# Kernel tuning notes

Hardware: AMD Instinct MI355X
Metric: run time of the kernel (lower is better)

Reference implementation:

```python
import jax, jax.numpy as jnp
import numpy as np
from jax import lax

N_ITERS = 32     # fixed iteration count (random graph diameter << 32, converges)
NEG = -1e9       # finite stand-in for -inf so grads stay finite


def _seg_logsumexp(x, seg, n):
    # numerically stable log-sum-exp scatter over segments (per-node over out-edges)
    m = jax.ops.segment_max(x, seg, num_segments=n)
    m = jnp.maximum(m, NEG)  # empty segments give -inf -> floor at NEG
    s = jax.ops.segment_sum(jnp.exp(x - m[seg]), seg, num_segments=n)
    return jnp.where(s > 0, jnp.log(s) + m, NEG)


def setup_inputs() -> dict:
    key = jax.random.key(0)
    k1, k2 = jax.random.split(key)
    N, E, F = 50000, 1600000, 64
    # scaled uniform features -> edge utilities ~ -7.4 mean => contraction, VI converges
    feats = jax.random.uniform(k1, (E, F), dtype=jnp.float32) * 0.2
    edge_index = jax.random.randint(k2, (2, E), 0, N)
    dest_mask = (jnp.arange(N) % 100) == 0  # 500 destination nodes
    batch = jnp.zeros((N,), dtype=jnp.int32)  # single graph (unused by VI solver)
    weight = jnp.full((1, F), -1.0, dtype=jnp.float32)  # module's constant init
    bias = jnp.full((1,), -1.0, dtype=jnp.float32)
    return {"feats": feats, "dest_mask": dest_mask, "edge_index": edge_index,
            "batch": batch, "n_nodes": N, "weight": weight, "bias": bias}


def reference(feats, dest_mask, edge_index, batch, n_nodes, weight, bias):
    # util = clamp(Linear(feats), -100, -1e-6), shape [E, 1]
    util = jnp.clip(feats @ weight.T + bias, -100.0, -1e-6)
    u = util[:, 0]                      # [E]
    src, dst = edge_index[0], edge_index[1]

    # value iteration: V(i) = LSE_{e: src(e)=i} (u_e + V(dst_e)), V(dest) = 0
    v0 = jnp.where(dest_mask, 0.0, NEG)

    def step(v, _):
        v_new = _seg_logsumexp(u + v[dst], src, n_nodes)
        v_new = jnp.where(dest_mask, 0.0, v_new)
        return v_new, None

    value, _ = lax.scan(step, v0, None, length=N_ITERS)  # [N]

    # edge choice probability: P(e) = exp(u_e + V(dst_e) - V(src_e))
    prob = jnp.exp(u + value[dst] - value[src])          # [E]
    return value, util, prob
```

## Files before the change

kernel.cpp:

```cpp
#include <hip/hip_runtime.h>

#define NEGV (-1000000000.0f)
#define N_ITERS 32
#define NBUCK 512
#define B1 256
#define REG 4096
#define CPAD 16

typedef float f32x4 __attribute__((ext_vector_type(4)));

__global__ __launch_bounds__(256) void util_kernel64gs(
    const float* __restrict__ feats, const float* __restrict__ weight,
    const float* __restrict__ bias, float* __restrict__ u,
    int* __restrict__ cursors, int* __restrict__ flags, int E)
{
    if (blockIdx.x == 0) {
        for (int i = threadIdx.x; i < NBUCK; i += 256)
            cursors[(size_t)i * CPAD] = i * REG;
        if (threadIdx.x <= N_ITERS)
            flags[threadIdx.x] = (threadIdx.x <= 1) ? 1 : 0;
    }
    int tid = blockIdx.x * blockDim.x + threadIdx.x;
    int l = tid & 15;
    int g = tid >> 4;
    int ngroups = (gridDim.x * blockDim.x) >> 4;
    f32x4 wv = *reinterpret_cast<const f32x4*>(weight + l * 4);
    float bb = bias[0];
    for (int e = g; e < E; e += ngroups) {
        f32x4 fv = __builtin_nontemporal_load(
            reinterpret_cast<const f32x4*>(feats + (size_t)e * 64 + l * 4));
        float s = fv.x * wv.x + fv.y * wv.y + fv.z * wv.z + fv.w * wv.w;
        s += __shfl_xor(s, 8, 16);
        s += __shfl_xor(s, 4, 16);
        s += __shfl_xor(s, 2, 16);
        s += __shfl_xor(s, 1, 16);
        if (l == 0)
            u[e] = fminf(fmaxf(s + bb, -100.0f), -1e-6f);
    }
}

__global__ __launch_bounds__(256) void util_kernel(
    const float* __restrict__ feats, const float* __restrict__ weight,
    const float* __restrict__ bias, float* __restrict__ u,
    int* __restrict__ cursors, int* __restrict__ flags, int E, int F)
{
    if (blockIdx.x == 0) {
        for (int i = threadIdx.x; i < NBUCK; i += 256)
            cursors[(size_t)i * CPAD] = i * REG;
        if (threadIdx.x <= N_ITERS)
            flags[threadIdx.x] = (threadIdx.x <= 1) ? 1 : 0;
    }
    int e = blockIdx.x * blockDim.x + threadIdx.x;
    if (e >= E) return;
    const float* row = feats + (size_t)e * (size_t)F;
    float acc = 0.0f;
    for (int f = 0; f < F; f += 4) {
        float4 fv = *reinterpret_cast<const float4*>(row + f);
        acc += fv.x * weight[f + 0];
        acc += fv.y * weight[f + 1];
        acc += fv.z * weight[f + 2];
        acc += fv.w * weight[f + 3];
    }
    acc += bias[0];
    u[e] = fminf(fmaxf(acc, -100.0f), -1e-6f);
}

__global__ __launch_bounds__(256) void scatter_fused(
    const int* __restrict__ src, const int* __restrict__ dst,
    const float* __restrict__ u, int* __restrict__ cursors,
    int2* __restrict__ edg, int E, int W, int chunk)
{
    __shared__ int h[NBUCK];
    for (int i = threadIdx.x; i < NBUCK; i += 256) h[i] = 0;
    __syncthreads();
    const int lo = blockIdx.x * chunk;
    const int hi = min(E, lo + chunk);
    for (int e = lo + threadIdx.x; e < hi; e += 256)
        atomicAdd(&h[(unsigned)src[e] / (unsigned)W], 1);
    __syncthreads();
    for (int k = threadIdx.x; k < NBUCK; k += 256) {
        int c = h[k];
        h[k] = (c > 0) ? atomicAdd(&cursors[(size_t)k * CPAD], c) : 0;
    }
    __syncthreads();
    for (int e = lo + threadIdx.x; e < hi; e += 256) {
        int s = src[e];
        unsigned k = (unsigned)s / (unsigned)W;
        int pos = atomicAdd(&h[k], 1);
        if (pos < (int)((k + 1) * REG)) {
            unsigned sl = (unsigned)s - k * (unsigned)W;
            int2 rec;
            rec.x = (int)((sl << 20) | (unsigned)dst[e]);
            rec.y = __float_as_int(expf(u[e]));
            edg[pos] = rec;
        }
    }
}

__global__ __launch_bounds__(256) void fine_sort(
    const int* __restrict__ cursors, int2* __restrict__ edg,
    int* __restrict__ row_ptr, int* __restrict__ row_end,
    const int* __restrict__ dest_mask, float* __restrict__ ew1,
    int N, int W)
{
    __shared__ int pks[REG];
    __shared__ int ubs[REG];
    __shared__ int fh[132];
    __shared__ int rst[132];

    const int k  = blockIdx.x;
    const int lo = k * W;
    const int nn = min(N, lo + W) - lo;
    if (nn <= 0) return;

    const int bs = k * REG;
    int cnt = cursors[(size_t)k * CPAD] - bs;
    if (cnt > REG) cnt = REG;
    if (cnt < 0) cnt = 0;

    for (int i = threadIdx.x; i < cnt; i += 256) {
        int2 r = edg[bs + i];
        pks[i] = r.x;
        ubs[i] = r.y;
    }
    for (int i = threadIdx.x; i < nn; i += 256) fh[i] = 0;
    __syncthreads();

    for (int i = threadIdx.x; i < cnt; i += 256)
        atomicAdd(&fh[((unsigned)pks[i]) >> 20], 1);
    __syncthreads();

    if (threadIdx.x == 0) {
        int run = bs;
        for (int i = 0; i < nn; ++i) {
            int c = fh[i];
            fh[i] = run;
            rst[i] = run;
            row_ptr[lo + i] = run;
            row_end[lo + i] = run + c;
            run += c;
        }
    }
    __syncthreads();

    for (int i = threadIdx.x; i < cnt; i += 256) {
        int w = pks[i];
        int pos = atomicAdd(&fh[((unsigned)w) >> 20], 1);
        int2 r;
        r.x = w & 0xFFFFF;
        r.y = ubs[i];
        edg[pos] = r;
    }
    __syncthreads();

    const int grp   = threadIdx.x >> 3;
    const int lane8 = threadIdx.x & 7;
    for (int base = 0; base < nn; base += 32) {
        int ridx = base + grp;
        if (ridx < nn) {
            int n  = lo + ridx;
            int rs = rst[ridx];
            int re = fh[ridx];
            float s = 0.0f;
            for (int j = rs + lane8; j < re; j += 8) {
                int2 r = edg[j];
                s += __int_as_float(r.y) * (dest_mask[r.x] ? 1.0f : 0.0f);
            }
            s += __shfl_xor(s, 4, 8);
            s += __shfl_xor(s, 2, 8);
            s += __shfl_xor(s, 1, 8);
            if (lane8 == 0)
                ew1[n] = dest_mask[n] ? 1.0f : s;
        }
    }
}

__global__ __launch_bounds__(256) void iter_exp_conv(
    const int* __restrict__ row_ptr, const int* __restrict__ row_end,
    const int2* __restrict__ edg, const int* __restrict__ dest_mask,
    const float* __restrict__ ew, float* __restrict__ ew_new,
    const int* __restrict__ flag_prev2, int* __restrict__ flag_cur, int N)
{
    __shared__ int blk_changed;
    int tid = blockIdx.x * blockDim.x + threadIdx.x;

    int2 fl = *reinterpret_cast<const int2*>(flag_prev2);
    if (fl.y == 0) {
        if (fl.x == 0) return;
        if (tid < N) ew_new[tid] = ew[tid];
        return;
    }

    if (threadIdx.x == 0) blk_changed = 0;
    __syncthreads();

    int n = tid >> 3;
    int lane8 = tid & 7;
    if (n < N) {
        int rs = row_ptr[n];
        int re = row_end[n];
        float s = 0.0f;
        for (int j = rs + lane8; j < re; j += 8) {
            int2 r = edg[j];
            s += __int_as_float(r.y) * ew[r.x];
        }
        s += __shfl_xor(s, 4, 8);
        s += __shfl_xor(s, 2, 8);
        s += __shfl_xor(s, 1, 8);
        if (lane8 == 0) {
            float nv = dest_mask[n] ? 1.0f : s;
            ew_new[n] = nv;
            if (__float_as_int(nv) != __float_as_int(ew[n])) blk_changed = 1;
        }
    }
    __syncthreads();
    if (threadIdx.x == 0 && blk_changed) atomicOr(flag_cur, 1);
}

__global__ __launch_bounds__(256) void final_exp_conv(
    const int* __restrict__ row_ptr, const int* __restrict__ row_end,
    const int2* __restrict__ edg, const int* __restrict__ dest_mask,
    const float* __restrict__ ew, float* __restrict__ value,
    const int* __restrict__ flag_prev, int N)
{
    int tid = blockIdx.x * blockDim.x + threadIdx.x;

    if (*flag_prev == 0) {
        if (tid < N) {
            float s = ew[tid];
            value[tid] = dest_mask[tid] ? 0.0f : (s > 0.0f ? logf(s) : NEGV);
        }
        return;
    }

    int n = tid >> 3;
    int lane8 = tid & 7;
    if (n >= N) return;
    int rs = row_ptr[n];
    int re = row_end[n];
    float s = 0.0f;
    for (int j = rs + lane8; j < re; j += 8) {
        int2 r = edg[j];
        s += __int_as_float(r.y) * ew[r.x];
    }
    s += __shfl_xor(s, 4, 8);
    s += __shfl_xor(s, 2, 8);
    s += __shfl_xor(s, 1, 8);
    if (lane8 == 0)
        value[n] = dest_mask[n] ? 0.0f : (s > 0.0f ? logf(s) : NEGV);
}

__global__ __launch_bounds__(256) void prob_kernel(
    const float* __restrict__ u, const int* __restrict__ src,
    const int* __restrict__ dst, const float* __restrict__ v,
    float* __restrict__ prob, int E)
{
    int e = blockIdx.x * blockDim.x + threadIdx.x;
    if (e >= E) return;
    prob[e] = expf((u[e] + v[dst[e]]) - v[src[e]]);
}

__global__ __launch_bounds__(256) void util_plain(
    const float* __restrict__ feats, const float* __restrict__ weight,
    const float* __restrict__ bias, float* __restrict__ u, int E, int F)
{
    int e = blockIdx.x * blockDim.x + threadIdx.x;
    if (e >= E) return;
    const float* row = feats + (size_t)e * (size_t)F;
    float acc = 0.0f;
    for (int f = 0; f < F; f += 4) {
        float4 fv = *reinterpret_cast<const float4*>(row + f);
        acc += fv.x * weight[f + 0];
        acc += fv.y * weight[f + 1];
        acc += fv.z * weight[f + 2];
        acc += fv.w * weight[f + 3];
    }
    acc += bias[0];
    u[e] = fminf(fmaxf(acc, -100.0f), -1e-6f);
}
__global__ __launch_bounds__(256) void init_pass(
    const int* __restrict__ dest_mask, float* v, float* s, int N)
{
    int n = blockIdx.x * blockDim.x + threadIdx.x;
    if (n >= N) return;
    v[n] = dest_mask[n] ? 0.0f : NEGV;
    s[n] = 0.0f;
}
__global__ __launch_bounds__(256) void edge_pass(
    const float* __restrict__ u, const int* __restrict__ src,
    const int* __restrict__ dst, const float* __restrict__ v, float* s, int E)
{
    int e = blockIdx.x * blockDim.x + threadIdx.x;
    if (e >= E) return;
    atomicAdd(&s[src[e]], expf(u[e] + v[dst[e]]));
}
__global__ __launch_bounds__(256) void node_pass(
    const int* __restrict__ dest_mask, float* v, float* s, int N)
{
    int n = blockIdx.x * blockDim.x + threadIdx.x;
    if (n >= N) return;
    float sv = s[n];
    v[n] = dest_mask[n] ? 0.0f : (sv > 0.0f ? logf(sv) : NEGV);
    s[n] = 0.0f;
}

extern "C" void kernel_launch(void* const* d_in, const int* in_sizes, int n_in,
                              void* d_out, int out_size, void* d_ws, size_t ws_size,
                              hipStream_t stream)
{
    const float* feats     = (const float*)d_in[0];
    const int*   dest_mask = (const int*)d_in[1];
    const int*   edge_index= (const int*)d_in[2];
    const float* weight    = (const float*)d_in[5];
    const float* bias      = (const float*)d_in[6];

    const int F = in_sizes[5];
    const int E = in_sizes[2] / 2;
    const int N = in_sizes[1];

    const int* src = edge_index;
    const int* dst = edge_index + E;

    float* out   = (float*)d_out;
    float* value = out;
    float* util  = out + N;
    float* prob  = out + (size_t)N + (size_t)E;

    const int eb = (E + 255) / 256;
    const int nb = (N + 255) / 256;

    const int W = (N + NBUCK - 1) / NBUCK;

    const size_t need_words = (size_t)NBUCK * CPAD + 2 * (size_t)NBUCK * REG
                            + 4 * (size_t)N + (N_ITERS + 1);
    const size_t need_bytes = need_words * 4;
    const bool pack_ok = (N < (1 << 20)) && (W <= 128)
                      && ((size_t)NBUCK * REG >= (size_t)E)
                      && ((N & 1) == 0);

    if (d_ws != nullptr && ws_size >= need_bytes && pack_ok) {
        int*   cursors = (int*)d_ws;
        int2*  edg     = (int2*)(cursors + (size_t)NBUCK * CPAD);
        int*   row_ptr = (int*)(edg + (size_t)NBUCK * REG);
        int*   row_end = row_ptr + N;
        float* ewa     = (float*)(row_end + N);
        float* ewb     = ewa + N;
        int*   flags   = (int*)(ewb + N);

        if (F == 64) {
            util_kernel64gs<<<2048, 256, 0, stream>>>(
                feats, weight, bias, util, cursors, flags, E);
        } else {
            util_kernel<<<eb, 256, 0, stream>>>(
                feats, weight, bias, util, cursors, flags, E, F);
        }

        const int chunk = (E + B1 - 1) / B1;
        scatter_fused<<<B1, 256, 0, stream>>>(src, dst, util, cursors, edg, E, W, chunk);
        fine_sort<<<NBUCK, 256, 0, stream>>>(
            cursors, edg, row_ptr, row_end, dest_mask, ewa, N, W);

        const int gb = ((N * 8) + 255) / 256;
        float* cur = ewa;
        float* nxt = ewb;
        for (int it = 2; it <= N_ITERS - 1; ++it) {
            iter_exp_conv<<<gb, 256, 0, stream>>>(
                row_ptr, row_end, edg, dest_mask, cur, nxt,
                flags + (it - 2), flags + it, N);
            float* t = cur; cur = nxt; nxt = t;
        }
        final_exp_conv<<<gb, 256, 0, stream>>>(
            row_ptr, row_end, edg, dest_mask, cur, value, flags + (N_ITERS - 1), N);

        prob_kernel<<<eb, 256, 0, stream>>>(util, src, dst, value, prob, E);
    } else {
        util_plain<<<eb, 256, 0, stream>>>(feats, weight, bias, util, E, F);
        float* s = prob;
        init_pass<<<nb, 256, 0, stream>>>(dest_mask, value, s, N);
        for (int it = 0; it < N_ITERS; ++it) {
            edge_pass<<<eb, 256, 0, stream>>>(util, src, dst, value, s, E);
            node_pass<<<nb, 256, 0, stream>>>(dest_mask, value, s, N);
        }
        prob_kernel<<<eb, 256, 0, stream>>>(util, src, dst, value, prob, E);
    }
}
```

Measured before the change: 361.6 us.

## Run tail value iterations in one cooperative persistent kernel with grid sync

Value iterations from IT_SPLIT onward now run inside a single cooperatively launched persistent kernel. Each iteration ends with a grid-wide sync and a check of the convergence flag, and the kernel breaks out early once nothing changes. This replaces up to 14 separate launches, removing per-launch overhead and the empty launches left after convergence. In exchange it adds device-attribute and occupancy queries on every call, the cost of grid.sync, and a persistent grid that may be smaller than the original launch. If the cooperative launch fails it falls back to the old per-iteration launches.

```diff
diff --git a/kernel.cpp b/kernel.cpp
--- a/kernel.cpp
+++ b/kernel.cpp
@@ -1,4 +1,7 @@
 #include <hip/hip_runtime.h>
+#include <hip/hip_cooperative_groups.h>
+
+namespace cg = cooperative_groups;
 
 #define NEGV (-1000000000.0f)
 #define N_ITERS 32
@@ -6,6 +9,7 @@
 #define B1 256
 #define REG 4096
 #define CPAD 16
+#define IT_SPLIT 18
 
 typedef float f32x4 __attribute__((ext_vector_type(4)));
 
@@ -217,6 +221,53 @@
     if (threadIdx.x == 0 && blk_changed) atomicOr(flag_cur, 1);
 }
 
+__global__ __launch_bounds__(256) void coop_tail(
+    const int* __restrict__ row_ptr, const int* __restrict__ row_end,
+    const int2* __restrict__ edg, const int* __restrict__ dest_mask,
+    float* cur0, float* nxt0, int* __restrict__ flags,
+    int N, int it_start, int it_end)
+{
+    if (flags[it_start - 1] == 0) return;
+
+    cg::grid_group grid = cg::this_grid();
+    __shared__ int fl_s;
+    const int tid = blockIdx.x * blockDim.x + threadIdx.x;
+    const int nthreads = gridDim.x * blockDim.x;
+    const int lane8 = tid & 7;
+    const int g0 = tid >> 3;
+    const int ngroups = nthreads >> 3;
+
+    float* cur = cur0;
+    float* nxt = nxt0;
+    for (int it = it_start; it <= it_end; ++it) {
+        int changed = 0;
+        for (int n = g0; n < N; n += ngroups) {
+            int rs = row_ptr[n];
+            int re = row_end[n];
+            float s = 0.0f;
+            for (int j = rs + lane8; j < re; j += 8) {
+                int2 r = edg[j];
+                s += __int_as_float(r.y) * cur[r.x];
+            }
+            s += __shfl_xor(s, 4, 8);
+            s += __shfl_xor(s, 2, 8);
+            s += __shfl_xor(s, 1, 8);
+            if (lane8 == 0) {
+                float nv = dest_mask[n] ? 1.0f : s;
+                nxt[n] = nv;
+                if (__float_as_int(nv) != __float_as_int(cur[n])) changed = 1;
+            }
+        }
+        if (changed) atomicOr(&flags[it], 1);
+        __threadfence();
+        grid.sync();
+        if (threadIdx.x == 0) fl_s = atomicOr(&flags[it], 0);
+        __syncthreads();
+        if (fl_s == 0) break;
+        float* t = cur; cur = nxt; nxt = t;
+    }
+}
+
 __global__ __launch_bounds__(256) void final_exp_conv(
     const int* __restrict__ row_ptr, const int* __restrict__ row_end,
     const int2* __restrict__ edg, const int* __restrict__ dest_mask,
@@ -363,11 +414,42 @@
         const int gb = ((N * 8) + 255) / 256;
         float* cur = ewa;
         float* nxt = ewb;
-        for (int it = 2; it <= N_ITERS - 1; ++it) {
+        for (int it = 2; it <= IT_SPLIT - 1; ++it) {
             iter_exp_conv<<<gb, 256, 0, stream>>>(
                 row_ptr, row_end, edg, dest_mask, cur, nxt,
                 flags + (it - 2), flags + it, N);
             float* t = cur; cur = nxt; nxt = t;
+        }
+        bool coop_done = false;
+        {
+            int dev = 0, coop = 0, numCU = 0, maxAct = 0;
+            hipGetDevice(&dev);
+            hipDeviceGetAttribute(&coop, hipDeviceAttributeCooperativeLaunch, dev);
+            hipDeviceGetAttribute(&numCU, hipDeviceAttributeMultiprocessorCount, dev);
+            hipOccupancyMaxActiveBlocksPerMultiprocessor(&maxAct,
+                reinterpret_cast<const void*>(coop_tail), 256, 0);
+            if (coop && maxAct >= 1 && numCU >= 1) {
+                int grid = maxAct * numCU;
+                if (grid > 2048) grid = 2048;
+                int it_start = IT_SPLIT, it_end = N_ITERS - 1;
+                void* args[] = {
+                    (void*)&row_ptr, (void*)&row_end, (void*)&edg, (void*)&dest_mask,
+                    (void*)&cur, (void*)&nxt, (void*)&flags,
+                    (void*)&N, (void*)&it_start, (void*)&it_end
+                };
+                hipError_t err = hipLaunchCooperativeKernel(
+                    reinterpret_cast<const void*>(coop_tail),
+                    dim3(grid), dim3(256), args, 0, stream);
+                coop_done = (err == hipSuccess);
+            }
+        }
+        if (!coop_done) {
+            for (int it = IT_SPLIT; it <= N_ITERS - 1; ++it) {
+                iter_exp_conv<<<gb, 256, 0, stream>>>(
+                    row_ptr, row_end, edg, dest_mask, cur, nxt,
+                    flags + (it - 2), flags + it, N);
+                float* t = cur; cur = nxt; nxt = t;
+            }
         }
         final_exp_conv<<<gb, 256, 0, stream>>>(
             row_ptr, row_end, edg, dest_mask, cur, value, flags + (N_ITERS - 1), N);
```

Result: slower. 378.5 us (+4.7%).
